# Kernel tuning notes

Hardware: AMD Instinct MI355X
Metric: run time of the kernel (lower is better)

Reference implementation:

```python
import jax, jax.numpy as jnp
import numpy as np

L = 3          # num_layers
D = 512        # hidden_dim
B, N = 8, 1024
EPS = 1e-5


def layernorm(x, gamma, beta):
    mu = jnp.mean(x, axis=-1, keepdims=True)
    var = jnp.var(x, axis=-1, keepdims=True)
    return (x - mu) * jax.lax.rsqrt(var + EPS) * gamma + beta


def setup_inputs() -> dict:
    key = jax.random.key(0)
    ks = jax.random.split(key, 12)
    s = 1.0 / np.sqrt(D)
    node_features = jax.random.normal(ks[0], (B, N, D), dtype=jnp.float32)
    adjacency_matrix = jax.random.randint(ks[1], (B, N, N), 0, 2, dtype=jnp.int32)
    return {
        "node_features": node_features,
        "adjacency_matrix": adjacency_matrix,
        # attn_linear: Linear(2D, 1) -> weight [2D], bias scalar, per layer
        "attn_w": jax.random.normal(ks[2], (L, 2 * D), dtype=jnp.float32) * (1.0 / np.sqrt(2 * D)),
        "attn_b": jax.random.normal(ks[3], (L,), dtype=jnp.float32) * 0.01,
        "W1": jax.random.normal(ks[4], (L, D, 4 * D), dtype=jnp.float32) * s,
        "b1": jnp.zeros((L, 4 * D), dtype=jnp.float32),
        "W2": jax.random.normal(ks[5], (L, 4 * D, D), dtype=jnp.float32) * (1.0 / np.sqrt(4 * D)),
        "b2": jnp.zeros((L, D), dtype=jnp.float32),
        "g1": jnp.ones((L, D), dtype=jnp.float32),
        "beta1": jnp.zeros((L, D), dtype=jnp.float32),
        "g2": jnp.ones((L, D), dtype=jnp.float32),
        "beta2": jnp.zeros((L, D), dtype=jnp.float32),
    }


def reference(node_features, adjacency_matrix, attn_w, attn_b, W1, b1, W2, b2, g1, beta1, g2, beta2):
    n = adjacency_matrix.shape[-1]
    # adjacency + self loops; mask of allowed edges
    mask = (adjacency_matrix.astype(jnp.float32) + jnp.eye(n, dtype=jnp.float32)) > 0  # [B,N,N]
    x = node_features
    d = x.shape[-1]
    for l in range(attn_w.shape[0]):
        # score_ij = a1.h_i + a2.h_j + b  (== Linear(concat(h_i,h_j)))
        si = x @ attn_w[l, :d]           # [B,N]
        sj = x @ attn_w[l, d:]           # [B,N]
        scores = si[:, :, None] + sj[:, None, :] + attn_b[l]   # [B,N,N]
        scores = jnp.where(scores >= 0, scores, 0.2 * scores)  # LeakyReLU(0.2)
        scores = jnp.where(mask, scores, -jnp.inf)
        attn = jax.nn.softmax(scores, axis=-1)                  # diag always unmasked
        agg = jnp.einsum('bij,bjd->bid', attn, x)
        h = layernorm(x + agg, g1[l], beta1[l])
        ff = jax.nn.gelu(h @ W1[l] + b1[l], approximate=False) @ W2[l] + b2[l]
        x = layernorm(h + ff, g2[l], beta2[l])
    return x
```

## Files before the change

### kernel.cpp

```cpp
#include <hip/hip_runtime.h>
#include <math.h>

#define NB 8
#define NN 1024
#define DD 512

typedef unsigned short u16;
typedef unsigned int u32;
typedef unsigned long long u64;
typedef __attribute__((ext_vector_type(8))) short bfrag;
typedef __attribute__((ext_vector_type(4))) float ffrag;

__device__ __forceinline__ u16 f2b(float f) {
    union { float f; u32 u; } v; v.f = f;
    u32 r = v.u + 0x7fffu + ((v.u >> 16) & 1u);
    return (u16)(r >> 16);
}
__device__ __forceinline__ float b2f(u16 b) {
    union { u32 u; float f; } v; v.u = ((u32)b) << 16;
    return v.f;
}

__device__ __forceinline__ float gelu_cheap(float v) {
    float s = v * 0.70710678118654752f;
    float a = fabsf(s);
    float t = 1.0f / (1.0f + 0.3275911f * a);
    float p = ((((1.061405429f * t - 1.453152027f) * t + 1.421413741f) * t
                - 0.284496736f) * t + 0.254829592f) * t;
    float erfa = 1.0f - p * __expf(-a * a);
    float erfs = copysignf(erfa, s);
    return 0.5f * v * (1.0f + erfs);
}

__device__ __forceinline__ void gload_lds16(const void* g, void* l) {
    __builtin_amdgcn_global_load_lds(
        (const __attribute__((address_space(1))) void*)g,
        (__attribute__((address_space(3))) void*)l, 16, 0, 0);
}

__global__ __launch_bounds__(256) void mask_pack(const int* __restrict__ adj,
                                                 u64* __restrict__ mb) {
    int idx = blockIdx.x * 256 + threadIdx.x;
    int w = idx & 15;
    int bi = idx >> 4;
    int i = bi & 1023;
    const int4* p = (const int4*)(adj + (size_t)bi * NN + w * 64);
    u64 m = 0;
#pragma unroll
    for (int q = 0; q < 16; ++q) {
        int4 v = p[q];
        if (v.x > 0) m |= 1ull << (q * 4 + 0);
        if (v.y > 0) m |= 1ull << (q * 4 + 1);
        if (v.z > 0) m |= 1ull << (q * 4 + 2);
        if (v.w > 0) m |= 1ull << (q * 4 + 3);
    }
    if (w == (i >> 6)) m |= 1ull << (i & 63);
    mb[idx] = m;
}

__global__ __launch_bounds__(256) void transpose_cvt(
    const float* __restrict__ in, u16* __restrict__ out,
    int R, int C, size_t inStr, size_t outStr)
{
    __shared__ float tile[32][33];
    int z = blockIdx.z;
    int r0 = blockIdx.y * 32, c0 = blockIdx.x * 32;
    int t = threadIdx.x;
    int tr = t >> 3, tc = (t & 7) * 4;
    float4 v = *(const float4*)(in + inStr * z + (size_t)(r0 + tr) * C + c0 + tc);
    tile[tr][tc + 0] = v.x; tile[tr][tc + 1] = v.y;
    tile[tr][tc + 2] = v.z; tile[tr][tc + 3] = v.w;
    __syncthreads();
    u32 w0 = (u32)f2b(tile[tc + 0][tr]) | ((u32)f2b(tile[tc + 1][tr]) << 16);
    u32 w1 = (u32)f2b(tile[tc + 2][tr]) | ((u32)f2b(tile[tc + 3][tr]) << 16);
    uint2 wv; wv.x = w0; wv.y = w1;
    *(uint2*)(out + outStr * z + (size_t)(c0 + tr) * R + r0 + tc) = wv;
}

__global__ __launch_bounds__(256) void score_proj_kernel(
    const float* __restrict__ x, const float* __restrict__ w,
    float* __restrict__ si, float* __restrict__ sj)
{
    int wave = threadIdx.x >> 6;
    int lane = threadIdx.x & 63;
    int row = blockIdx.x * 4 + wave;
    const float4* xr = (const float4*)(x + (size_t)row * DD) + lane * 2;
    const float4* w1 = (const float4*)(w) + lane * 2;
    const float4* w2 = (const float4*)(w + DD) + lane * 2;
    float a = 0.f, b2 = 0.f;
#pragma unroll
    for (int c = 0; c < 2; ++c) {
        float4 xv = xr[c], wa = w1[c], wb = w2[c];
        a  += xv.x * wa.x + xv.y * wa.y + xv.z * wa.z + xv.w * wa.w;
        b2 += xv.x * wb.x + xv.y * wb.y + xv.z * wb.z + xv.w * wb.w;
    }
#pragma unroll
    for (int off = 32; off > 0; off >>= 1) {
        a  += __shfl_xor(a, off);
        b2 += __shfl_xor(b2, off);
    }
    if (lane == 0) { si[row] = a; sj[row] = b2; }
}

__global__ __launch_bounds__(256) void softmax_p(
    const float* __restrict__ si, const float* __restrict__ sj,
    const float* __restrict__ attn_b, const u64* __restrict__ mb,
    u16* __restrict__ P)
{
    __shared__ u16 sb[8 * NN];
    int b  = blockIdx.x >> 7;
    int i0 = (blockIdx.x & 127) * 8;
    int tid = threadIdx.x;
    int r = tid >> 5, l32 = tid & 31;
    int i = i0 + r;
    float bb = attn_b[0];
    float siv = si[b * NN + i];
    const float* sjb = sj + b * NN;
    const u64* mbr = mb + ((size_t)b * NN + i) * 16;

    float sv[32];
    float mx = -INFINITY;
#pragma unroll
    for (int q = 0; q < 32; ++q) {
        int j = q * 32 + l32;
        u64 w = mbr[q >> 1];
        int bit = ((q & 1) << 5) + l32;
        float s = siv + sjb[j] + bb;
        s = (s >= 0.f) ? s : 0.2f * s;
        s = ((w >> bit) & 1ull) ? s : -INFINITY;
        sv[q] = s;
        mx = fmaxf(mx, s);
    }
#pragma unroll
    for (int off = 16; off > 0; off >>= 1) mx = fmaxf(mx, __shfl_xor(mx, off, 32));
    float sum = 0.f;
#pragma unroll
    for (int q = 0; q < 32; ++q) {
        float p = __expf(sv[q] - mx);
        sv[q] = p;
        sum += p;
    }
#pragma unroll
    for (int off = 16; off > 0; off >>= 1) sum += __shfl_xor(sum, off, 32);
    float inv = 1.f / sum;
#pragma unroll
    for (int q = 0; q < 32; ++q)
        sb[r * NN + q * 32 + l32] = f2b(sv[q] * inv);
    __syncthreads();
    const uint4* src = (const uint4*)sb;
    uint4* dst = (uint4*)(P + ((size_t)b * NN + i0) * NN);
#pragma unroll
    for (int t = 0; t < 4; ++t) dst[t * 256 + tid] = src[t * 256 + tid];
}

template <int EPI>
__global__ __launch_bounds__(256) void gemm64(
    const u16* __restrict__ A, const u16* __restrict__ Bm,
    const float* __restrict__ bias, const void* __restrict__ res,
    void* __restrict__ Cout, int K, int N, int lda, int ldb,
    size_t aStr, size_t bStr, size_t cStr, size_t resStr)
{
    __shared__ __align__(16) u16 lds[24576];
    int z = blockIdx.z;
    int m0 = blockIdx.y * 64, n0 = blockIdx.x * 128;
    int tid = threadIdx.x;
    int lane = tid & 63, wv = tid >> 6;

    const u16* ag[2]; const u16* bg[4];
    u32 la[2], lb[4];
#pragma unroll
    for (int i = 0; i < 2; ++i) {
        int q = i * 256 + tid;
        int row = q >> 3, c = q & 7;
        ag[i] = A + aStr * z + (size_t)(m0 + row) * lda + (c ^ (row & 7)) * 8;
        la[i] = i * 2048 + wv * 512;
    }
#pragma unroll
    for (int i = 0; i < 4; ++i) {
        int q = i * 256 + tid;
        int row = q >> 3, c = q & 7;
        bg[i] = Bm + bStr * z + (size_t)(n0 + row) * ldb + (c ^ (row & 7)) * 8;
        lb[i] = 8192 + i * 2048 + wv * 512;
    }

    int mw = (wv >> 1) * 32, nw = (wv & 1) * 64;
    int lr = lane & 15, lq = lane >> 4;
    int sw = lr & 7;

    ffrag acc[2][4];
#pragma unroll
    for (int i = 0; i < 2; ++i)
#pragma unroll
        for (int j = 0; j < 4; ++j) acc[i][j] = (ffrag){0.f, 0.f, 0.f, 0.f};

#pragma unroll
    for (int i = 0; i < 2; ++i) gload_lds16(ag[i], &lds[la[i]]);
#pragma unroll
    for (int i = 0; i < 4; ++i) gload_lds16(bg[i], &lds[lb[i]]);

    for (int k0 = 0; k0 < K; k0 += 64) {
        int cur = (k0 >> 6) & 1;
        if (k0 + 64 < K) {
#pragma unroll
            for (int i = 0; i < 2; ++i)
                gload_lds16(ag[i] + k0 + 64, &lds[((cur ^ 1) << 12) + la[i]]);
#pragma unroll
            for (int i = 0; i < 4; ++i)
                gload_lds16(bg[i] + k0 + 64, &lds[((cur ^ 1) << 13) + lb[i]]);
            asm volatile("s_waitcnt vmcnt(6)" ::: "memory");
        } else {
            asm volatile("s_waitcnt vmcnt(0)" ::: "memory");
        }
        asm volatile("s_barrier" ::: "memory");

        const u16* Ab = &lds[cur << 12];
        const u16* Bb = &lds[8192 + (cur << 13)];
#pragma unroll
        for (int h = 0; h < 2; ++h) {
            bfrag af[2], bf[4];
#pragma unroll
            for (int i = 0; i < 2; ++i)
                af[i] = *(const bfrag*)&Ab[(mw + i * 16 + lr) * 64 + ((h * 4 + lq) ^ sw) * 8];
#pragma unroll
            for (int j = 0; j < 4; ++j)
                bf[j] = *(const bfrag*)&Bb[(nw + j * 16 + lr) * 64 + ((h * 4 + lq) ^ sw) * 8];
#pragma unroll
            for (int i = 0; i < 2; ++i)
#pragma unroll
                for (int j = 0; j < 4; ++j)
                    acc[i][j] = __builtin_amdgcn_mfma_f32_16x16x32_bf16(af[i], bf[j], acc[i][j], 0, 0, 0);
        }
        asm volatile("s_waitcnt lgkmcnt(0)\ns_barrier" ::: "memory");
    }

    float* Cf = (float*)Cout + cStr * z;
    u16*   Cb = (u16*)Cout + cStr * z;
    const float* resf = (const float*)res;
    const u16*   resb = (const u16*)res;
#pragma unroll
    for (int i = 0; i < 2; ++i) {
        int row = m0 + mw + i * 16 + lq * 4;
#pragma unroll
        for (int j = 0; j < 4; ++j) {
            int col = n0 + nw + j * 16 + lr;
            float bv = (EPI != 0) ? bias[col] : 0.f;
#pragma unroll
            for (int r = 0; r < 4; ++r) {
                float v = acc[i][j][r] + bv;
                size_t off = (size_t)(row + r) * N + col;
                if (EPI == 1) {
                    Cb[off] = f2b(gelu_cheap(v));
                } else if (EPI == 0) {
                    Cf[off] = v + resf[resStr * z + off];
                } else {
                    Cf[off] = v + b2f(resb[off]);
                }
            }
        }
    }
}

template <bool BF>
__global__ __launch_bounds__(256) void ln_kernel(
    const float* __restrict__ in, const float* __restrict__ g,
    const float* __restrict__ be, void* __restrict__ out)
{
    int row = blockIdx.x;
    int tid = threadIdx.x;
    const float2* rp = (const float2*)(in + (size_t)row * DD);
    float2 v = rp[tid];
    float s  = v.x + v.y;
    float ss = v.x * v.x + v.y * v.y;
#pragma unroll
    for (int off = 32; off > 0; off >>= 1) {
        s  += __shfl_xor(s, off);
        ss += __shfl_xor(ss, off);
    }
    __shared__ float sh[8];
    int wave = tid >> 6, lane = tid & 63;
    if (lane == 0) { sh[wave] = s; sh[4 + wave] = ss; }
    __syncthreads();
    float S  = sh[0] + sh[1] + sh[2] + sh[3];
    float SS = sh[4] + sh[5] + sh[6] + sh[7];
    float mean = S * (1.f / DD);
    float var  = SS * (1.f / DD) - mean * mean;
    var = fmaxf(var, 0.f);
    float rs = rsqrtf(var + 1e-5f);
    float2 gv = ((const float2*)g)[tid];
    float2 bv = ((const float2*)be)[tid];
    float ox = (v.x - mean) * rs * gv.x + bv.x;
    float oy = (v.y - mean) * rs * gv.y + bv.y;
    if (BF) {
        u32 w = (u32)f2b(ox) | ((u32)f2b(oy) << 16);
        ((u32*)out)[(size_t)row * (DD / 2) + tid] = w;
    } else {
        float2 o; o.x = ox; o.y = oy;
        ((float2*)out)[(size_t)row * (DD / 2) + tid] = o;
    }
}

extern "C" void kernel_launch(void* const* d_in, const int* in_sizes, int n_in,
                              void* d_out, int out_size, void* d_ws, size_t ws_size,
                              hipStream_t stream) {
    const float* nf     = (const float*)d_in[0];
    const int*   adj    = (const int*)d_in[1];
    const float* attn_w = (const float*)d_in[2];
    const float* attn_b = (const float*)d_in[3];
    const float* W1     = (const float*)d_in[4];
    const float* b1     = (const float*)d_in[5];
    const float* W2     = (const float*)d_in[6];
    const float* b2     = (const float*)d_in[7];
    const float* g1     = (const float*)d_in[8];
    const float* be1    = (const float*)d_in[9];
    const float* g2     = (const float*)d_in[10];
    const float* be2    = (const float*)d_in[11];
    float* out = (float*)d_out;

    char* wsb = (char*)d_ws;
    float* x_cur = (float*)(wsb);
    u16*   h_bf  = (u16*)(wsb + 16777216);
    char*  scr   = wsb + 25165824;
    u16*   P     = (u16*)scr;
    float* hres  = (float*)(scr + 16777216);
    u16*   mid   = (u16*)scr;
    u16*   xT    = (u16*)(wsb + 58720256);
    u16*   W1t   = (u16*)(wsb + 67108864);
    u16*   W2t   = (u16*)(wsb + 73400320);
    u64*   mask  = (u64*)(wsb + 79691776);
    float* si    = (float*)(wsb + 80740352);
    float* sj    = (float*)(wsb + 80773120);

    mask_pack<<<512, 256, 0, stream>>>(adj, mask);
    transpose_cvt<<<dim3(64, 16, 3), 256, 0, stream>>>(W1, W1t, 512, 2048,
                                                       (size_t)512 * 2048, (size_t)512 * 2048);
    transpose_cvt<<<dim3(16, 64, 3), 256, 0, stream>>>(W2, W2t, 2048, 512,
                                                       (size_t)2048 * 512, (size_t)2048 * 512);

    for (int l = 0; l < 3; ++l) {
        const float* xin = (l == 0) ? nf : x_cur;
        score_proj_kernel<<<2048, 256, 0, stream>>>(xin, attn_w + (size_t)l * 1024, si, sj);
        transpose_cvt<<<dim3(16, 32, 8), 256, 0, stream>>>(xin, xT, 1024, 512,
                                                           (size_t)NN * DD, (size_t)NN * DD);
        softmax_p<<<1024, 256, 0, stream>>>(si, sj, attn_b + l, mask, P);
        gemm64<0><<<dim3(4, 16, 8), 256, 0, stream>>>(
            P, xT, nullptr, xin, hres, 1024, 512, 1024, 1024,
            (size_t)NN * NN, (size_t)DD * NN, (size_t)NN * DD, (size_t)NN * DD);
        ln_kernel<true><<<8192, 256, 0, stream>>>(hres, g1 + (size_t)l * 512, be1 + (size_t)l * 512, h_bf);
        gemm64<1><<<dim3(16, 128, 1), 256, 0, stream>>>(
            h_bf, W1t + (size_t)l * 1048576, b1 + (size_t)l * 2048, nullptr, mid,
            512, 2048, 512, 512, 0, 0, 0, 0);
        gemm64<2><<<dim3(4, 128, 1), 256, 0, stream>>>(
            mid, W2t + (size_t)l * 1048576, b2 + (size_t)l * 512, h_bf, x_cur,
            2048, 512, 2048, 2048, 0, 0, 0, 0);
        void* lnout = (l == 2) ? (void*)out : (void*)x_cur;
        ln_kernel<false><<<8192, 256, 0, stream>>>(x_cur, g2 + (size_t)l * 512, be2 + (size_t)l * 512, lnout);
    }
}
```

Measured before the change: 476.0 us.

## Fuse next-layer score projection into LayerNorm and use 128x128 tiles for FFN1

Adds a 128x128-tile double-buffered bf16 MFMA GEMM kernel and uses it for the first FFN matmul (512->2048), replacing the 64-wide tile variant to increase data reuse per block. Also fuses the next layer's attention score projections (si, sj) into the second LayerNorm kernel, removing a separate pass over x for layers 1 and 2. The larger tile uses more LDS and registers and launches fewer blocks, which may reduce occupancy.

```diff
diff --git a/kernel.cpp b/kernel.cpp
--- a/kernel.cpp
+++ b/kernel.cpp
@@ -239,6 +239,109 @@
     const u16*   resb = (const u16*)res;
 #pragma unroll
     for (int i = 0; i < 2; ++i) {
+        int row = m0 + mw + i * 16 + lq * 4;
+#pragma unroll
+        for (int j = 0; j < 4; ++j) {
+            int col = n0 + nw + j * 16 + lr;
+            float bv = (EPI != 0) ? bias[col] : 0.f;
+#pragma unroll
+            for (int r = 0; r < 4; ++r) {
+                float v = acc[i][j][r] + bv;
+                size_t off = (size_t)(row + r) * N + col;
+                if (EPI == 1) {
+                    Cb[off] = f2b(gelu_cheap(v));
+                } else if (EPI == 0) {
+                    Cf[off] = v + resf[resStr * z + off];
+                } else {
+                    Cf[off] = v + b2f(resb[off]);
+                }
+            }
+        }
+    }
+}
+
+template <int EPI>
+__global__ __launch_bounds__(256) void gemm128p(
+    const u16* __restrict__ A, const u16* __restrict__ Bm,
+    const float* __restrict__ bias, const void* __restrict__ res,
+    void* __restrict__ Cout, int K, int N, int lda, int ldb,
+    size_t aStr, size_t bStr, size_t cStr, size_t resStr)
+{
+    __shared__ __align__(16) u16 lds[32768];
+    int z = blockIdx.z;
+    int m0 = blockIdx.y * 128, n0 = blockIdx.x * 128;
+    int tid = threadIdx.x;
+    int lane = tid & 63, wv = tid >> 6;
+
+    const u16* ag[4]; const u16* bg[4];
+    u32 la[4], lb[4];
+#pragma unroll
+    for (int i = 0; i < 4; ++i) {
+        int q = i * 256 + tid;
+        int row = q >> 3, c = q & 7;
+        int gc = c ^ (row & 7);
+        ag[i] = A  + aStr * z + (size_t)(m0 + row) * lda + gc * 8;
+        bg[i] = Bm + bStr * z + (size_t)(n0 + row) * ldb + gc * 8;
+        la[i] = i * 2048 + wv * 512;
+        lb[i] = 16384 + i * 2048 + wv * 512;
+    }
+
+    int mw = (wv >> 1) * 64, nw = (wv & 1) * 64;
+    int lr = lane & 15, lq = lane >> 4;
+    int sw = lr & 7;
+
+    ffrag acc[4][4];
+#pragma unroll
+    for (int i = 0; i < 4; ++i)
+#pragma unroll
+        for (int j = 0; j < 4; ++j) acc[i][j] = (ffrag){0.f, 0.f, 0.f, 0.f};
+
+#pragma unroll
+    for (int i = 0; i < 4; ++i) gload_lds16(ag[i], &lds[la[i]]);
+#pragma unroll
+    for (int i = 0; i < 4; ++i) gload_lds16(bg[i], &lds[lb[i]]);
+
+    for (int k0 = 0; k0 < K; k0 += 64) {
+        int cur = (k0 >> 6) & 1;
+        if (k0 + 64 < K) {
+#pragma unroll
+            for (int i = 0; i < 4; ++i)
+                gload_lds16(ag[i] + k0 + 64, &lds[((cur ^ 1) << 13) + la[i]]);
+#pragma unroll
+            for (int i = 0; i < 4; ++i)
+                gload_lds16(bg[i] + k0 + 64, &lds[((cur ^ 1) << 13) + lb[i]]);
+            asm volatile("s_waitcnt vmcnt(8)" ::: "memory");
+        } else {
+            asm volatile("s_waitcnt vmcnt(0)" ::: "memory");
+        }
+        asm volatile("s_barrier" ::: "memory");
+
+        const u16* Ab = &lds[cur << 13];
+        const u16* Bb = &lds[16384 + (cur << 13)];
+#pragma unroll
+        for (int h = 0; h < 2; ++h) {
+            bfrag af[4], bf[4];
+#pragma unroll
+            for (int i = 0; i < 4; ++i)
+                af[i] = *(const bfrag*)&Ab[(mw + i * 16 + lr) * 64 + ((h * 4 + lq) ^ sw) * 8];
+#pragma unroll
+            for (int j = 0; j < 4; ++j)
+                bf[j] = *(const bfrag*)&Bb[(nw + j * 16 + lr) * 64 + ((h * 4 + lq) ^ sw) * 8];
+#pragma unroll
+            for (int i = 0; i < 4; ++i)
+#pragma unroll
+                for (int j = 0; j < 4; ++j)
+                    acc[i][j] = __builtin_amdgcn_mfma_f32_16x16x32_bf16(af[i], bf[j], acc[i][j], 0, 0, 0);
+        }
+        asm volatile("s_waitcnt lgkmcnt(0)\ns_barrier" ::: "memory");
+    }
+
+    float* Cf = (float*)Cout + cStr * z;
+    u16*   Cb = (u16*)Cout + cStr * z;
+    const float* resf = (const float*)res;
+    const u16*   resb = (const u16*)res;
+#pragma unroll
+    for (int i = 0; i < 4; ++i) {
         int row = m0 + mw + i * 16 + lq * 4;
 #pragma unroll
         for (int j = 0; j < 4; ++j) {
@@ -299,6 +402,56 @@
     }
 }
 
+__global__ __launch_bounds__(256) void ln2_score(
+    const float* __restrict__ in, const float* __restrict__ g,
+    const float* __restrict__ be, const float* __restrict__ wnx,
+    float* __restrict__ xout, float* __restrict__ si, float* __restrict__ sj)
+{
+    int row = blockIdx.x;
+    int tid = threadIdx.x;
+    const float2* rp = (const float2*)(in + (size_t)row * DD);
+    float2 v = rp[tid];
+    float s  = v.x + v.y;
+    float ss = v.x * v.x + v.y * v.y;
+#pragma unroll
+    for (int off = 32; off > 0; off >>= 1) {
+        s  += __shfl_xor(s, off);
+        ss += __shfl_xor(ss, off);
+    }
+    __shared__ float sh[16];
+    int wave = tid >> 6, lane = tid & 63;
+    if (lane == 0) { sh[wave] = s; sh[4 + wave] = ss; }
+    __syncthreads();
+    float S  = sh[0] + sh[1] + sh[2] + sh[3];
+    float SS = sh[4] + sh[5] + sh[6] + sh[7];
+    float mean = S * (1.f / DD);
+    float var  = SS * (1.f / DD) - mean * mean;
+    var = fmaxf(var, 0.f);
+    float rs = rsqrtf(var + 1e-5f);
+    float2 gv = ((const float2*)g)[tid];
+    float2 bv = ((const float2*)be)[tid];
+    float ox = (v.x - mean) * rs * gv.x + bv.x;
+    float oy = (v.y - mean) * rs * gv.y + bv.y;
+    float2 o; o.x = ox; o.y = oy;
+    ((float2*)xout)[(size_t)row * (DD / 2) + tid] = o;
+
+    float2 wa = ((const float2*)wnx)[tid];
+    float2 wb = ((const float2*)(wnx + DD))[tid];
+    float a = ox * wa.x + oy * wa.y;
+    float b = ox * wb.x + oy * wb.y;
+#pragma unroll
+    for (int off = 32; off > 0; off >>= 1) {
+        a += __shfl_xor(a, off);
+        b += __shfl_xor(b, off);
+    }
+    if (lane == 0) { sh[8 + wave] = a; sh[12 + wave] = b; }
+    __syncthreads();
+    if (tid == 0) {
+        si[row] = sh[8] + sh[9] + sh[10] + sh[11];
+        sj[row] = sh[12] + sh[13] + sh[14] + sh[15];
+    }
+}
+
 extern "C" void kernel_launch(void* const* d_in, const int* in_sizes, int n_in,
                               void* d_out, int out_size, void* d_ws, size_t ws_size,
                               hipStream_t stream) {
@@ -338,7 +491,8 @@
 
     for (int l = 0; l < 3; ++l) {
         const float* xin = (l == 0) ? nf : x_cur;
-        score_proj_kernel<<<2048, 256, 0, stream>>>(xin, attn_w + (size_t)l * 1024, si, sj);
+        if (l == 0)
+            score_proj_kernel<<<2048, 256, 0, stream>>>(xin, attn_w, si, sj);
         transpose_cvt<<<dim3(16, 32, 8), 256, 0, stream>>>(xin, xT, 1024, 512,
                                                            (size_t)NN * DD, (size_t)NN * DD);
         softmax_p<<<1024, 256, 0, stream>>>(si, sj, attn_b + l, mask, P);
@@ -346,13 +500,20 @@
             P, xT, nullptr, xin, hres, 1024, 512, 1024, 1024,
             (size_t)NN * NN, (size_t)DD * NN, (size_t)NN * DD, (size_t)NN * DD);
         ln_kernel<true><<<8192, 256, 0, stream>>>(hres, g1 + (size_t)l * 512, be1 + (size_t)l * 512, h_bf);
-        gemm64<1><<<dim3(16, 128, 1), 256, 0, stream>>>(
+        gemm128p<1><<<dim3(16, 64, 1), 256, 0, stream>>>(
             h_bf, W1t + (size_t)l * 1048576, b1 + (size_t)l * 2048, nullptr, mid,
             512, 2048, 512, 512, 0, 0, 0, 0);
         gemm64<2><<<dim3(4, 128, 1), 256, 0, stream>>>(
             mid, W2t + (size_t)l * 1048576, b2 + (size_t)l * 512, h_bf, x_cur,
             2048, 512, 2048, 2048, 0, 0, 0, 0);
-        void* lnout = (l == 2) ? (void*)out : (void*)x_cur;
-        ln_kernel<false><<<8192, 256, 0, stream>>>(x_cur, g2 + (size_t)l * 512, be2 + (size_t)l * 512, lnout);
-    }
-}
+        if (l == 2) {
+            ln_kernel<false><<<8192, 256, 0, stream>>>(x_cur, g2 + (size_t)l * 512,
+                                                       be2 + (size_t)l * 512, out);
+        } else {
+            ln2_score<<<8192, 256, 0, stream>>>(x_cur, g2 + (size_t)l * 512,
+                                                be2 + (size_t)l * 512,
+                                                attn_w + (size_t)(l + 1) * 1024,
+                                                x_cur, si, sj);
+        }
+    }
+}
```

After: 479.8 us. About the same (+0.8%).

## Use 128x128 double-buffered MFMA tile for FFN up-projection and merge weight transposes

Applied to the files above, without the earlier changes.

Replaces the 64-tile GEMM for the W1 up-projection (with GELU epilogue) with a new 128x128 block-tile kernel. Each wave computes a 64x64 sub-tile using bf16 MFMA and double-buffered direct global-to-LDS loads with an XOR swizzle. This raises arithmetic intensity per LDS load and cuts the number of blocks. It also fuses the two weight transpose launches into one kernel to save a launch. Risks are higher register pressure and lower occupancy from the 64 accumulators per lane, and fewer blocks (1024) to fill the GPU.

```diff
diff --git a/kernel.cpp b/kernel.cpp
--- a/kernel.cpp
+++ b/kernel.cpp
@@ -56,6 +56,34 @@
     }
     if (w == (i >> 6)) m |= 1ull << (i & 63);
     mb[idx] = m;
+}
+
+__global__ __launch_bounds__(256) void wtrans(
+    const float* __restrict__ W1, const float* __restrict__ W2,
+    u16* __restrict__ W1t, u16* __restrict__ W2t)
+{
+    __shared__ float tile[32][33];
+    int z = blockIdx.y;
+    int bid = blockIdx.x;
+    const float* in; u16* out; int R, C, c0, r0;
+    if (z < 3) {
+        in = W1 + (size_t)z * 512 * 2048; out = W1t + (size_t)z * 1048576;
+        R = 512; C = 2048; c0 = (bid & 63) * 32; r0 = (bid >> 6) * 32;
+    } else {
+        int l = z - 3;
+        in = W2 + (size_t)l * 2048 * 512; out = W2t + (size_t)l * 1048576;
+        R = 2048; C = 512; c0 = (bid & 15) * 32; r0 = (bid >> 4) * 32;
+    }
+    int t = threadIdx.x;
+    int tr = t >> 3, tc = (t & 7) * 4;
+    float4 v = *(const float4*)(in + (size_t)(r0 + tr) * C + c0 + tc);
+    tile[tr][tc + 0] = v.x; tile[tr][tc + 1] = v.y;
+    tile[tr][tc + 2] = v.z; tile[tr][tc + 3] = v.w;
+    __syncthreads();
+    u32 w0 = (u32)f2b(tile[tc + 0][tr]) | ((u32)f2b(tile[tc + 1][tr]) << 16);
+    u32 w1 = (u32)f2b(tile[tc + 2][tr]) | ((u32)f2b(tile[tc + 3][tr]) << 16);
+    uint2 wv; wv.x = w0; wv.y = w1;
+    *(uint2*)(out + (size_t)(c0 + tr) * R + r0 + tc) = wv;
 }
 
 __global__ __launch_bounds__(256) void transpose_cvt(
@@ -255,6 +283,92 @@
                 } else {
                     Cf[off] = v + b2f(resb[off]);
                 }
+            }
+        }
+    }
+}
+
+__global__ __launch_bounds__(256) void gemm128d(
+    const u16* __restrict__ A, const u16* __restrict__ Bm,
+    const float* __restrict__ bias, u16* __restrict__ Cout,
+    int K, int N, int lda, int ldb)
+{
+    __shared__ __align__(16) u16 lds[16384];
+    int m0 = blockIdx.y * 128, n0 = blockIdx.x * 128;
+    int tid = threadIdx.x;
+    int lane = tid & 63, wv = tid >> 6;
+
+    const u16* ag[2]; const u16* bg[2];
+    u32 la[2], lb[2];
+#pragma unroll
+    for (int i = 0; i < 2; ++i) {
+        int q = i * 256 + tid;
+        int row = q >> 2, c = q & 3;
+        int gc = c ^ (row & 3);
+        ag[i] = A  + (size_t)(m0 + row) * lda + gc * 8;
+        bg[i] = Bm + (size_t)(n0 + row) * ldb + gc * 8;
+        la[i] = i * 2048 + wv * 512;
+        lb[i] = 8192 + i * 2048 + wv * 512;
+    }
+
+    int mw = (wv >> 1) * 64, nw = (wv & 1) * 64;
+    int lr = lane & 15, lq = lane >> 4;
+    int sw = lr & 3;
+
+    ffrag acc[4][4];
+#pragma unroll
+    for (int i = 0; i < 4; ++i)
+#pragma unroll
+        for (int j = 0; j < 4; ++j) acc[i][j] = (ffrag){0.f, 0.f, 0.f, 0.f};
+
+#pragma unroll
+    for (int i = 0; i < 2; ++i) gload_lds16(ag[i], &lds[la[i]]);
+#pragma unroll
+    for (int i = 0; i < 2; ++i) gload_lds16(bg[i], &lds[lb[i]]);
+
+    for (int k0 = 0; k0 < K; k0 += 32) {
+        int cur = (k0 >> 5) & 1;
+        if (k0 + 32 < K) {
+#pragma unroll
+            for (int i = 0; i < 2; ++i)
+                gload_lds16(ag[i] + k0 + 32, &lds[(cur ^ 1) * 4096 + la[i]]);
+#pragma unroll
+            for (int i = 0; i < 2; ++i)
+                gload_lds16(bg[i] + k0 + 32, &lds[(cur ^ 1) * 4096 + lb[i]]);
+            asm volatile("s_waitcnt vmcnt(4)" ::: "memory");
+        } else {
+            asm volatile("s_waitcnt vmcnt(0)" ::: "memory");
+        }
+        asm volatile("s_barrier" ::: "memory");
+
+        const u16* Ab = &lds[cur * 4096];
+        const u16* Bb = &lds[8192 + cur * 4096];
+        bfrag af[4], bf[4];
+#pragma unroll
+        for (int i = 0; i < 4; ++i)
+            af[i] = *(const bfrag*)&Ab[(mw + i * 16 + lr) * 32 + (lq ^ sw) * 8];
+#pragma unroll
+        for (int j = 0; j < 4; ++j)
+            bf[j] = *(const bfrag*)&Bb[(nw + j * 16 + lr) * 32 + (lq ^ sw) * 8];
+#pragma unroll
+        for (int i = 0; i < 4; ++i)
+#pragma unroll
+            for (int j = 0; j < 4; ++j)
+                acc[i][j] = __builtin_amdgcn_mfma_f32_16x16x32_bf16(af[i], bf[j], acc[i][j], 0, 0, 0);
+        asm volatile("s_waitcnt lgkmcnt(0)\ns_barrier" ::: "memory");
+    }
+
+#pragma unroll
+    for (int i = 0; i < 4; ++i) {
+        int row = m0 + mw + i * 16 + lq * 4;
+#pragma unroll
+        for (int j = 0; j < 4; ++j) {
+            int col = n0 + nw + j * 16 + lr;
+            float bv = bias[col];
+#pragma unroll
+            for (int r = 0; r < 4; ++r) {
+                float v = acc[i][j][r] + bv;
+                Cout[(size_t)(row + r) * N + col] = f2b(gelu_cheap(v));
             }
         }
     }
@@ -331,10 +445,7 @@
     float* sj    = (float*)(wsb + 80773120);
 
     mask_pack<<<512, 256, 0, stream>>>(adj, mask);
-    transpose_cvt<<<dim3(64, 16, 3), 256, 0, stream>>>(W1, W1t, 512, 2048,
-                                                       (size_t)512 * 2048, (size_t)512 * 2048);
-    transpose_cvt<<<dim3(16, 64, 3), 256, 0, stream>>>(W2, W2t, 2048, 512,
-                                                       (size_t)2048 * 512, (size_t)2048 * 512);
+    wtrans<<<dim3(1024, 6), 256, 0, stream>>>(W1, W2, W1t, W2t);
 
     for (int l = 0; l < 3; ++l) {
         const float* xin = (l == 0) ? nf : x_cur;
@@ -346,9 +457,8 @@
             P, xT, nullptr, xin, hres, 1024, 512, 1024, 1024,
             (size_t)NN * NN, (size_t)DD * NN, (size_t)NN * DD, (size_t)NN * DD);
         ln_kernel<true><<<8192, 256, 0, stream>>>(hres, g1 + (size_t)l * 512, be1 + (size_t)l * 512, h_bf);
-        gemm64<1><<<dim3(16, 128, 1), 256, 0, stream>>>(
-            h_bf, W1t + (size_t)l * 1048576, b1 + (size_t)l * 2048, nullptr, mid,
-            512, 2048, 512, 512, 0, 0, 0, 0);
+        gemm128d<<<dim3(16, 64), 256, 0, stream>>>(
+            h_bf, W1t + (size_t)l * 1048576, b1 + (size_t)l * 2048, mid, 512, 2048, 512, 512);
         gemm64<2><<<dim3(4, 128, 1), 256, 0, stream>>>(
             mid, W2t + (size_t)l * 1048576, b2 + (size_t)l * 512, h_bf, x_cur,
             2048, 512, 2048, 2048, 0, 0, 0, 0);
```

After: 480.8 us. About the same (+1.0%).
